# Kernel tuning notes

Hardware: AMD Instinct MI355X
Metric: run time of the kernel (lower is better)

The kernel has to match this reference:

```python
import jax, jax.numpy as jnp
from jax import lax
import numpy as np

T, B, I, H, O = 512, 64, 512, 1024, 512


def setup_inputs() -> dict:
    key = jax.random.key(0)
    ks = jax.random.split(key, 8)
    s_ih = 1.0 / np.sqrt(I)
    s_hh = 1.0 / np.sqrt(H)
    return {
        "x": jax.random.normal(ks[0], (T, B, I), dtype=jnp.float32),
        "hidden": jnp.zeros((1, B, H), dtype=jnp.float32),
        "W_ih": jax.random.normal(ks[1], (H, I), dtype=jnp.float32) * s_ih,
        "W_hh": jax.random.normal(ks[2], (H, H), dtype=jnp.float32) * s_hh,
        "b_ih": jax.random.normal(ks[3], (H,), dtype=jnp.float32) * s_hh,
        "b_hh": jax.random.normal(ks[4], (H,), dtype=jnp.float32) * s_hh,
        "W_fc": jax.random.normal(ks[5], (O, H), dtype=jnp.float32) * s_hh,
        "b_fc": jax.random.normal(ks[6], (O,), dtype=jnp.float32) * s_hh,
    }


def reference(x, hidden, W_ih, W_hh, b_ih, b_hh, W_fc, b_fc):
    # Precompute the input projection for all timesteps as one big GEMM.
    # xp: [T, B, H]
    xp = jnp.einsum("tbi,hi->tbh", x, W_ih) + b_ih

    h0 = hidden[0]  # [B, H]

    def step(h, xt):
        # PyTorch RNN (tanh): h_t = tanh(W_ih x_t + b_ih + W_hh h_{t-1} + b_hh)
        h_new = jnp.tanh(xt + h @ W_hh.T + b_hh)
        return h_new, h_new

    h_last, hs = lax.scan(step, h0, xp)  # hs: [T, B, H]

    # fc applied to flattened [T*B, H] hidden states
    out = hs.reshape(-1, hs.shape[-1]) @ W_fc.T + b_fc  # [T*B, O]
    return out, h_last[None]  # ([T*B, O], [1, B, H])
```

## Files before the change

kernel.cpp:

```cpp
#include <hip/hip_runtime.h>

typedef __attribute__((ext_vector_type(8))) short bf16x8;
typedef __attribute__((ext_vector_type(4))) float f32x4;

#define T_N 512
#define I_N 512
#define H_N 1024
#define O_N 512
#define NCL 4
#define NMEM 16
#define NTHR 512
#define COLS_H 64
#define KW 192
#define AP_STRIDE 1544
#define RST 9
#define CANARY 0xFFFFFFFFu
#define HS_CAP 20000000
#define POLL_CAP 200000

__device__ __forceinline__ unsigned short f2bf(float f) {
  unsigned int u = __float_as_uint(f);
  u += 0x7fffu + ((u >> 16) & 1u);
  return (unsigned short)(u >> 16);
}
__device__ __forceinline__ bf16x8 cvt8f(const float* __restrict__ p) {
  float4 a = *(const float4*)p;
  float4 b = *(const float4*)(p + 4);
  bf16x8 r;
  r[0] = (short)f2bf(a.x); r[1] = (short)f2bf(a.y);
  r[2] = (short)f2bf(a.z); r[3] = (short)f2bf(a.w);
  r[4] = (short)f2bf(b.x); r[5] = (short)f2bf(b.y);
  r[6] = (short)f2bf(b.z); r[7] = (short)f2bf(b.w);
  return r;
}
__device__ __forceinline__ bf16x8 cvt8v(float4 a, float4 b) {
  bf16x8 r;
  r[0] = (short)f2bf(a.x); r[1] = (short)f2bf(a.y);
  r[2] = (short)f2bf(a.z); r[3] = (short)f2bf(a.w);
  r[4] = (short)f2bf(b.x); r[5] = (short)f2bf(b.y);
  r[6] = (short)f2bf(b.z); r[7] = (short)f2bf(b.w);
  return r;
}

__device__ __forceinline__ void barrier_lds() {
  asm volatile("s_waitcnt lgkmcnt(0)" ::: "memory");
  __builtin_amdgcn_s_barrier();
  __builtin_amdgcn_sched_barrier(0);
}

__device__ __forceinline__ void st_sc01(unsigned int* p, unsigned int v) {
  asm volatile("global_store_dword %0, %1, off sc0 sc1" :: "v"(p), "v"(v) : "memory");
}
__device__ __forceinline__ void st_raw32(unsigned int* p, unsigned int v) {
  asm volatile("global_store_dword %0, %1, off" :: "v"(p), "v"(v) : "memory");
}
__device__ __forceinline__ unsigned int ld_sc01(const unsigned int* p) {
  unsigned int r;
  asm volatile("global_load_dword %0, %1, off sc0 sc1\n\ts_waitcnt vmcnt(0)"
               : "=v"(r) : "v"(p) : "memory");
  return r;
}
__device__ __forceinline__ void ld_sc01_rw(unsigned int* d, const unsigned int* p) {
  asm volatile("global_load_dword %0, %1, off sc0 sc1" : "+v"(*d) : "v"(p) : "memory");
}
__device__ __forceinline__ void ld_sc01_nw(unsigned int* d, const unsigned int* p) {
  asm volatile("global_load_dword %0, %1, off sc0 sc1" : "=v"(*d) : "v"(p) : "memory");
}
__device__ __forceinline__ void ld4_rawf(float4* d, const void* p) {
  asm volatile("global_load_dwordx4 %0, %1, off" : "=v"(*d) : "v"(p) : "memory");
}

#define PHASE(G, X0, X1, X2, X3)                                               \
  {                                                                            \
    const bool doSweep = !((G) == 0 && t == 0) && !((G) == 1 && t == T_N - 1); \
    unsigned int sw[8];                                                        \
    const unsigned int* spd = ringc;                                           \
    if (doSweep) {                                                             \
      const int swt = t - 1 + (G);                                             \
      spd = ringc + (((G) ^ 1) * 4 + (swt & 3)) * 4096 + tid;                  \
      _Pragma("unroll")                                                        \
      for (int j = 0; j < 8; ++j) {                                            \
        sw[j] = CANARY;                                                        \
        ld_sc01_rw(&sw[j], spd + 512 * j);                                     \
      }                                                                        \
    }                                                                          \
                     \
    f32x4 acc0 = {}, acc1 = {}, acc2 = {}, acc3 = {};                          \
    const int abase = (l & 15) * AP_STRIDE + wv * KW + ((l >> 4) << 3);        \
    _Pragma("unroll")                                                          \
    for (int kst = 0; kst < 6; ++kst) {                                        \
      bf16x8 a = *(const bf16x8*)(Apan + abase + kst * 32);                    \
      acc0 = __builtin_amdgcn_mfma_f32_16x16x32_bf16(a, Bh[kst][0], acc0,0,0,0);\
      acc1 = __builtin_amdgcn_mfma_f32_16x16x32_bf16(a, Bh[kst][1], acc1,0,0,0);\
      acc2 = __builtin_amdgcn_mfma_f32_16x16x32_bf16(a, Bh[kst][2], acc2,0,0,0);\
      acc3 = __builtin_amdgcn_mfma_f32_16x16x32_bf16(a, Bh[kst][3], acc3,0,0,0);\
    }                                                                          \
    if ((l >> 5) == (G)) {      \
      const int rb = ((l >> 4) & 1) << 2;                                      \
      *(f32x4*)(R + (size_t)(wv * COLS_H +  0 + (l & 15)) * RST + rb) = acc0;  \
      *(f32x4*)(R + (size_t)(wv * COLS_H + 16 + (l & 15)) * RST + rb) = acc1;  \
      *(f32x4*)(R + (size_t)(wv * COLS_H + 32 + (l & 15)) * RST + rb) = acc2;  \
      *(f32x4*)(R + (size_t)(wv * COLS_H + 48 + (l & 15)) * RST + rb) = acc3;  \
    }                                                                          \
    barrier_lds();            \
    if (wv < 4) {                                                              \
      float v0 = pb0, v1 = pb1;                                                \
      _Pragma("unroll")                                                        \
      for (int kk = 0; kk < 8; ++kk) {                                         \
        v0 += R[(size_t)(kk * COLS_H + 2 * rcp)     * RST + rrow];             \
        v1 += R[(size_t)(kk * COLS_H + 2 * rcp + 1) * RST + rrow];             \
      }                                                                        \
      const float h0 = tanhf(v0), h1 = tanhf(v1);                              \
      const unsigned int pk =                                                  \
          (unsigned int)f2bf(h0) | ((unsigned int)f2bf(h1) << 16);             \
                             \
      st_sc01(ringc + ((G) * 4 + (t & 3)) * 4096 + pubdw, pk);                 \
      st_sc01(ringc + ((G) * 4 + ((t + 2) & 3)) * 4096 + pubdw, CANARY);       \
      st_raw32((unsigned int*)(hs + ((size_t)t * 64 + b0 + (G) * 8 + rrow) * H_N \
                               + cbh + 2 * rcp), pk);                          \
      if (doSweep) {                                                           \
        asm volatile("s_waitcnt vmcnt(3)" ::: "memory");                       \
        __builtin_amdgcn_sched_barrier(0);                                     \
        bool bad = false;                                                      \
        _Pragma("unroll")                                                      \
        for (int j = 0; j < 8; ++j) bad |= (sw[j] == CANARY);                  \
        if (bad) {                                                             \
          int it = 0;                                                          \
          do {                                                                 \
            _Pragma("unroll")                                                  \
            for (int j = 0; j < 8; ++j) ld_sc01_nw(&sw[j], spd + 512 * j);     \
            asm volatile("s_waitcnt vmcnt(0)" ::: "memory");                   \
            __builtin_amdgcn_sched_barrier(0);                                 \
            bad = false;                                                       \
            _Pragma("unroll")                                                  \
            for (int j = 0; j < 8; ++j) bad |= (sw[j] == CANARY);              \
          } while (bad && ++it < POLL_CAP);                                    \
        }                                                                      \
      }                                                                        \
      if (t == T_N - 1) {                                                      \
        float2 fv; fv.x = h0; fv.y = h1;                                       \
        *(float2*)(hlast + (size_t)(b0 + (G) * 8 + rrow) * H_N + cbh + 2 * rcp) = fv; \
      }                                                                        \
    } else {                                                                   \
      if (t + 1 < T_N) {   \
        const int u = tid & 255;                                               \
        *(bf16x8*)(Apan + ((G) * 8 + (u >> 6)) * AP_STRIDE + H_N + ((u & 63) << 3)) = \
            cvt8v(X0, X1);                                                     \
        *(bf16x8*)(Apan + ((G) * 8 + (u >> 6) + 4) * AP_STRIDE + H_N + ((u & 63) << 3)) = \
            cvt8v(X2, X3);                                                     \
      }                                                                        \
      int nIss = 0;                                                            \
      if (t + 2 < T_N) {                               \
        const int u = tid & 255;                                               \
        const float* px = x + ((size_t)(t + 2) * 64 + b0 + (G) * 8 + (u >> 6)) * I_N \
                          + ((u & 63) << 3);                                   \
        ld4_rawf(&X0, px); ld4_rawf(&X1, px + 4);                              \
        ld4_rawf(&X2, px + 4 * I_N); ld4_rawf(&X3, px + 4 * I_N + 4);          \
        nIss = 4;                                                              \
      }                                                                        \
      if (doSweep) {                                                           \
        if (nIss) asm volatile("s_waitcnt vmcnt(4)" ::: "memory");             \
        else      asm volatile("s_waitcnt vmcnt(0)" ::: "memory");             \
        __builtin_amdgcn_sched_barrier(0);                                     \
        bool bad = false;                                                      \
        _Pragma("unroll")                                                      \
        for (int j = 0; j < 8; ++j) bad |= (sw[j] == CANARY);                  \
        if (bad) {                                                             \
          int it = 0;                                                          \
          do {                                                                 \
            _Pragma("unroll")                                                  \
            for (int j = 0; j < 8; ++j) ld_sc01_nw(&sw[j], spd + 512 * j);     \
            asm volatile("s_waitcnt vmcnt(0)" ::: "memory");                   \
            __builtin_amdgcn_sched_barrier(0);                                 \
            bad = false;                                                       \
            _Pragma("unroll")                                                  \
            for (int j = 0; j < 8; ++j) bad |= (sw[j] == CANARY);              \
          } while (bad && ++it < POLL_CAP);                                    \
        }                                                                      \
      }                                                                        \
    }                                                                          \
    if (doSweep) {     \
      _Pragma("unroll")                                                        \
      for (int j = 0; j < 8; ++j)                                              \
        *(unsigned int*)(Apan + ((((G) ^ 1) * 8) + j) * AP_STRIDE + (tid << 1)) = sw[j]; \
    }                                                                          \
    barrier_lds();                                   \
  }

__global__ __launch_bounds__(NTHR, 2) void rnn_scan(
    const float* __restrict__ x, const float* __restrict__ hidden,
    const float* __restrict__ Wih, const float* __restrict__ Whh,
    const float* __restrict__ bih, const float* __restrict__ bhh,
    unsigned short* __restrict__ hs, float* __restrict__ hlast,
    unsigned int* __restrict__ ring, unsigned int* __restrict__ flags)
{
  __shared__ __align__(16) unsigned short Apan[16 * AP_STRIDE];
  __shared__ __align__(16) float R[8 * COLS_H * RST];

  const int tid = threadIdx.x;
  const int l = tid & 63, wv = tid >> 6;
  const int bid = blockIdx.x;
  const int c = bid & 3;
  const int m = bid >> 2;
  const int b0 = c * 16;
  const int cbh = m * COLS_H;
  unsigned int* ringc = ring + (size_t)c * 2 * 4 * 4096;
  unsigned int* bar = flags + c * 64;

  bf16x8 Bh[6][4];
  {
    const int kb0 = wv * KW + ((l >> 4) << 3);
#pragma unroll
    for (int kst = 0; kst < 6; ++kst) {
      const int k = kb0 + kst * 32;
#pragma unroll
      for (int f = 0; f < 4; ++f) {
        const int col = cbh + f * 16 + (l & 15);
        const float* src = (k < H_N) ? (Whh + (size_t)col * H_N + k)
                                     : (Wih + (size_t)col * I_N + (k - H_N));
        Bh[kst][f] = cvt8f(src);
      }
    }
  }
  const int rrow = (tid >> 5) & 7;
  const int rcp  = tid & 31;
  const float pb0 = bih[cbh + 2 * rcp]     + bhh[cbh + 2 * rcp];
  const float pb1 = bih[cbh + 2 * rcp + 1] + bhh[cbh + 2 * rcp + 1];
  const int pubdw = rrow * 512 + m * 32 + rcp;

  {
    int q = tid;
#pragma unroll
    for (int i = 0; i < 4; ++i, q += NTHR) {
      const int row = q >> 7, col8 = (q & 127) << 3;
      *(bf16x8*)(Apan + row * AP_STRIDE + col8) =
          cvt8f(hidden + (size_t)(b0 + row) * H_N + col8);
    }
  }
  {
    int q = tid;
#pragma unroll
    for (int i = 0; i < 2; ++i, q += NTHR) {
      const int row = q >> 6, col8 = (q & 63) << 3;
      *(bf16x8*)(Apan + row * AP_STRIDE + H_N + col8) =
          cvt8f(x + (size_t)(b0 + row) * I_N + col8);
    }
  }
  if (tid < 256) {
#pragma unroll
    for (int s = 0; s < 8; ++s) st_sc01(ringc + s * 4096 + pubdw, CANARY);
  }
  asm volatile("s_waitcnt vmcnt(0)" ::: "memory");
  __syncthreads();
  if (tid == 0) st_sc01(&bar[m], 1u);
  if (tid < NMEM) {
    int it = 0;
    while (ld_sc01(&bar[tid]) < 1u && ++it < HS_CAP)
      if (it > 64) __builtin_amdgcn_s_sleep(1);
  }
  float4 xA0, xA1, xA2, xA3, xB0, xB1, xB2, xB3;
  if (wv >= 4) {
    const int u = tid & 255;
    const float* pa = x + (size_t)(64 + b0 + (u >> 6)) * I_N + ((u & 63) << 3);
    ld4_rawf(&xA0, pa); ld4_rawf(&xA1, pa + 4);
    ld4_rawf(&xA2, pa + 4 * I_N); ld4_rawf(&xA3, pa + 4 * I_N + 4);
    const float* pb = x + (size_t)(64 + b0 + 8 + (u >> 6)) * I_N + ((u & 63) << 3);
    ld4_rawf(&xB0, pb); ld4_rawf(&xB1, pb + 4);
    ld4_rawf(&xB2, pb + 4 * I_N); ld4_rawf(&xB3, pb + 4 * I_N + 4);
  }
  __syncthreads();

  for (int t = 0; t < T_N; ++t) {
    PHASE(0, xA0, xA1, xA2, xA3)
    PHASE(1, xB0, xB1, xB2, xB3)
  }
}

__global__ __launch_bounds__(256) void gemm_fc(const unsigned short* __restrict__ A,
                                               const unsigned short* __restrict__ Bt,
                                               const float* __restrict__ bias,
                                               float* __restrict__ C) {
  const int N = O_N, K = H_N;
  const int bm = blockIdx.x >> 2, bn = blockIdx.x & 3;
  const int l = threadIdx.x & 63, w = threadIdx.x >> 6;
  const int wr = w >> 1, wc = w & 1;
  const int row_a = bm * 128 + wr * 64 + (l & 15);
  const int row_b = bn * 128 + wc * 64 + (l & 15);
  const int koff = (l >> 4) * 8;
  f32x4 acc[4][4] = {};
  for (int k = 0; k < K; k += 32) {
    bf16x8 a[4], b[4];
#pragma unroll
    for (int i = 0; i < 4; i++)
      a[i] = *(const bf16x8*)(A + (size_t)(row_a + i * 16) * K + k + koff);
#pragma unroll
    for (int i = 0; i < 4; i++)
      b[i] = *(const bf16x8*)(Bt + (size_t)(row_b + i * 16) * K + k + koff);
#pragma unroll
    for (int i = 0; i < 4; i++)
#pragma unroll
      for (int j = 0; j < 4; j++)
        acc[i][j] = __builtin_amdgcn_mfma_f32_16x16x32_bf16(a[i], b[j], acc[i][j], 0, 0, 0);
  }
  const int orow = bm * 128 + wr * 64 + ((l >> 4) << 2);
  const int ocol = bn * 128 + wc * 64 + (l & 15);
#pragma unroll
  for (int i = 0; i < 4; i++)
#pragma unroll
    for (int j = 0; j < 4; j++) {
      const int r0 = orow + i * 16, c0 = ocol + j * 16;
      const float bv = bias[c0];
#pragma unroll
      for (int r = 0; r < 4; r++)
        C[(size_t)(r0 + r) * N + c0] = acc[i][j][r] + bv;
    }
}

__global__ __launch_bounds__(256) void cvt8(const float* __restrict__ s,
                                            unsigned short* __restrict__ d, long n) {
  long i = ((long)blockIdx.x * blockDim.x + threadIdx.x) * 8;
  if (i < n) *(bf16x8*)(d + i) = cvt8f(s + i);
}

extern "C" void kernel_launch(void* const* d_in, const int* in_sizes, int n_in,
                              void* d_out, int out_size, void* d_ws, size_t ws_size,
                              hipStream_t stream) {
  const float* x   = (const float*)d_in[0];
  const float* hid = (const float*)d_in[1];
  const float* Wih = (const float*)d_in[2];
  const float* Whh = (const float*)d_in[3];
  const float* bih = (const float*)d_in[4];
  const float* bhh = (const float*)d_in[5];
  const float* Wfc = (const float*)d_in[6];
  const float* bfc = (const float*)d_in[7];

  float* out   = (float*)d_out;
  float* hlast = out + (size_t)32768 * 512;

  unsigned int*   flags = (unsigned int*)d_ws;
  unsigned int*   ring  = (unsigned int*)((char*)d_ws + 4096);
  unsigned short* Wfcb  = (unsigned short*)((char*)d_ws + 4096 + 524288);
  unsigned short* hsb   = Wfcb + (size_t)512 * 1024;

  (void)hipMemsetAsync(flags, 0, 4096, stream);
  cvt8<<<256, 256, 0, stream>>>(Wfc, Wfcb, (long)512 * 1024);
  rnn_scan<<<64, NTHR, 0, stream>>>(x, hid, Wih, Whh, bih, bhh, hsb, hlast, ring, flags);
  gemm_fc<<<1024, 256, 0, stream>>>(hsb, Wfcb, bfc, out);
}
```

Before: 1.638 ms.

## Split recurrent step into four 4-row phases with deeper ring pipelining

Each block's 16 batch rows are now processed in four phases of 4 rows instead of two phases of 8, with a four-group ring buffer so a group's hidden state is published and consumed further ahead of its use. The reduction is restructured: 256 threads each produce one column value, packed via a lane shuffle before publishing. The x-staging loads are rotated across phases. A large LDS pad array is added, apparently to cap occupancy at one block per CU. The intent is to shorten the critical path per recurrent step by overlapping inter-block communication with MFMA work. The cost is twice as many barriers per timestep and more complex wait-count bookkeeping.

```diff
diff --git a/kernel.cpp b/kernel.cpp
--- a/kernel.cpp
+++ b/kernel.cpp
@@ -13,7 +13,7 @@
 #define COLS_H 64
 #define KW 192
 #define AP_STRIDE 1544
-#define RST 9
+#define SLOTDW 2048
 #define CANARY 0xFFFFFFFFu
 #define HS_CAP 20000000
 #define POLL_CAP 200000
@@ -70,121 +70,102 @@
   asm volatile("global_load_dwordx4 %0, %1, off" : "=v"(*d) : "v"(p) : "memory");
 }
 
-#define PHASE(G, X0, X1, X2, X3)                                               \
+#define PHASE(G, BISS, BCHK, XS0, XS1, XI0, XI1)                               \
   {                                                                            \
-    const bool doSweep = !((G) == 0 && t == 0) && !((G) == 1 && t == T_N - 1); \
-    unsigned int sw[8];                                                        \
-    const unsigned int* spd = ringc;                                           \
-    if (doSweep) {                                                             \
-      const int swt = t - 1 + (G);                                             \
-      spd = ringc + (((G) ^ 1) * 4 + (swt & 3)) * 4096 + tid;                  \
+    const bool iss  = ((G) == 0) ? (t >= 1) : (t <= 510);                      \
+    const bool chk  = ((G) == 3) ? (t <= 510) : (t >= 1);                      \
+    const int  tp   = ((G) == 0) ? (t - 1) : t;                                \
+    const int  tpp  = ((G) == 3) ? (t + 1) : t;                                \
+    const bool xiss = ((G) == 3) ? (t <= 509) : (t <= 510);                    \
+    const bool xstg = (t <= 510);                                              \
+    if (tid < 256) {                                                           \
+      if (iss) {                                                               \
+        const unsigned int* sb =                                               \
+            ringc + ((((G) + 3) & 3) * 4 + (tp & 3)) * SLOTDW + tid;           \
+        _Pragma("unroll")                                                      \
+        for (int q = 0; q < 8; ++q) {                                          \
+          BISS[q] = CANARY;                                                    \
+          ld_sc01_rw(&BISS[q], sb + 256 * q);                                  \
+        }                                                                      \
+      }                                                                        \
+    } else if (xiss) {                                                         \
+      const int u = tid & 255;                                                 \
+      const float* px = x + ((size_t)(tpp + 1) * 64 + b0 + 4 * (((G) + 1) & 3) \
+                             + (u >> 6)) * I_N + ((u & 63) << 3);              \
+      ld4_rawf(&XI0, px); ld4_rawf(&XI1, px + 4);                              \
+    }                                                                          \
+                                    \
+    {                                                                          \
+      f32x4 acc0 = {}, acc1 = {}, acc2 = {}, acc3 = {};                        \
+      const int abase = (l & 15) * AP_STRIDE + wv * KW + ((l >> 4) << 3);      \
       _Pragma("unroll")                                                        \
-      for (int j = 0; j < 8; ++j) {                                            \
-        sw[j] = CANARY;                                                        \
-        ld_sc01_rw(&sw[j], spd + 512 * j);                                     \
+      for (int kst = 0; kst < 6; ++kst) {                                      \
+        bf16x8 a = *(const bf16x8*)(Apan + abase + kst * 32);                  \
+        acc0 = __builtin_amdgcn_mfma_f32_16x16x32_bf16(a, Bh[kst][0], acc0, 0, 0, 0); \
+        acc1 = __builtin_amdgcn_mfma_f32_16x16x32_bf16(a, Bh[kst][1], acc1, 0, 0, 0); \
+        acc2 = __builtin_amdgcn_mfma_f32_16x16x32_bf16(a, Bh[kst][2], acc2, 0, 0, 0); \
+        acc3 = __builtin_amdgcn_mfma_f32_16x16x32_bf16(a, Bh[kst][3], acc3, 0, 0, 0); \
+      }                                                                        \
+      if ((l >> 4) == (G)) {             \
+        float* rb = Rbuf + wv * 256 + (l & 15) * 4;                            \
+        *(f32x4*)(rb +   0) = acc0; *(f32x4*)(rb +  64) = acc1;                \
+        *(f32x4*)(rb + 128) = acc2; *(f32x4*)(rb + 192) = acc3;                \
       }                                                                        \
     }                                                                          \
-                     \
-    f32x4 acc0 = {}, acc1 = {}, acc2 = {}, acc3 = {};                          \
-    const int abase = (l & 15) * AP_STRIDE + wv * KW + ((l >> 4) << 3);        \
-    _Pragma("unroll")                                                          \
-    for (int kst = 0; kst < 6; ++kst) {                                        \
-      bf16x8 a = *(const bf16x8*)(Apan + abase + kst * 32);                    \
-      acc0 = __builtin_amdgcn_mfma_f32_16x16x32_bf16(a, Bh[kst][0], acc0,0,0,0);\
-      acc1 = __builtin_amdgcn_mfma_f32_16x16x32_bf16(a, Bh[kst][1], acc1,0,0,0);\
-      acc2 = __builtin_amdgcn_mfma_f32_16x16x32_bf16(a, Bh[kst][2], acc2,0,0,0);\
-      acc3 = __builtin_amdgcn_mfma_f32_16x16x32_bf16(a, Bh[kst][3], acc3,0,0,0);\
-    }                                                                          \
-    if ((l >> 5) == (G)) {      \
-      const int rb = ((l >> 4) & 1) << 2;                                      \
-      *(f32x4*)(R + (size_t)(wv * COLS_H +  0 + (l & 15)) * RST + rb) = acc0;  \
-      *(f32x4*)(R + (size_t)(wv * COLS_H + 16 + (l & 15)) * RST + rb) = acc1;  \
-      *(f32x4*)(R + (size_t)(wv * COLS_H + 32 + (l & 15)) * RST + rb) = acc2;  \
-      *(f32x4*)(R + (size_t)(wv * COLS_H + 48 + (l & 15)) * RST + rb) = acc3;  \
-    }                                                                          \
-    barrier_lds();            \
-    if (wv < 4) {                                                              \
-      float v0 = pb0, v1 = pb1;                                                \
+    barrier_lds();          \
+    if (tid < 256) {                                                           \
+      float v = pbv;                                                           \
       _Pragma("unroll")                                                        \
-      for (int kk = 0; kk < 8; ++kk) {                                         \
-        v0 += R[(size_t)(kk * COLS_H + 2 * rcp)     * RST + rrow];             \
-        v1 += R[(size_t)(kk * COLS_H + 2 * rcp + 1) * RST + rrow];             \
-      }                                                                        \
-      const float h0 = tanhf(v0), h1 = tanhf(v1);                              \
-      const unsigned int pk =                                                  \
-          (unsigned int)f2bf(h0) | ((unsigned int)f2bf(h1) << 16);             \
-                             \
-      st_sc01(ringc + ((G) * 4 + (t & 3)) * 4096 + pubdw, pk);                 \
-      st_sc01(ringc + ((G) * 4 + ((t + 2) & 3)) * 4096 + pubdw, CANARY);       \
-      st_raw32((unsigned int*)(hs + ((size_t)t * 64 + b0 + (G) * 8 + rrow) * H_N \
-                               + cbh + 2 * rcp), pk);                          \
-      if (doSweep) {                                                           \
-        asm volatile("s_waitcnt vmcnt(3)" ::: "memory");                       \
+      for (int kk = 0; kk < 8; ++kk) v += Rbuf[kk * 256 + tid];                \
+      const float hval = tanhf(v);                                             \
+      const unsigned int pk16 = f2bf(hval);                                    \
+      const unsigned int oth = (unsigned int)__shfl_xor((int)pk16, 4);         \
+      if (!(tid & 4)) {                                                        \
+        const unsigned int pk = pk16 | (oth << 16);                            \
+        const int dwi = (tid & 3) * 512 + m * 32 + (tid >> 3);                 \
+        st_sc01(ringc + ((G) * 4 + (t & 3)) * SLOTDW + dwi, pk);               \
+        st_sc01(ringc + ((G) * 4 + ((t + 2) & 3)) * SLOTDW + dwi, CANARY);     \
+        st_raw32((unsigned int*)hs +                                           \
+                 ((size_t)t * 64 + b0 + 4 * (G) + (tid & 3)) * 512 +           \
+                 m * 32 + (tid >> 3), pk);                                     \
+      }                                                                        \
+      if (t == T_N - 1)                                                        \
+        hlast[(size_t)(b0 + 4 * (G) + (tid & 3)) * H_N + cbh + (tid >> 2)] = hval; \
+      if (chk) {                                                               \
+        asm volatile("s_waitcnt vmcnt(25)" ::: "memory");                      \
         __builtin_amdgcn_sched_barrier(0);                                     \
         bool bad = false;                                                      \
         _Pragma("unroll")                                                      \
-        for (int j = 0; j < 8; ++j) bad |= (sw[j] == CANARY);                  \
-        if (bad) {                                                             \
-          int it = 0;                                                          \
+        for (int q = 0; q < 8; ++q) bad |= (BCHK[q] == CANARY);                \
+        if (bad) {    \
+          const int ts = ((G) == 3) ? t : (t - 1);                             \
+          const unsigned int* sb2 =                                            \
+              ringc + ((((G) + 1) & 3) * 4 + (ts & 3)) * SLOTDW + tid;         \
+          int itc = 0;                                                         \
           do {                                                                 \
             _Pragma("unroll")                                                  \
-            for (int j = 0; j < 8; ++j) ld_sc01_nw(&sw[j], spd + 512 * j);     \
+            for (int q = 0; q < 8; ++q) ld_sc01_nw(&BCHK[q], sb2 + 256 * q);   \
             asm volatile("s_waitcnt vmcnt(0)" ::: "memory");                   \
             __builtin_amdgcn_sched_barrier(0);                                 \
             bad = false;                                                       \
             _Pragma("unroll")                                                  \
-            for (int j = 0; j < 8; ++j) bad |= (sw[j] == CANARY);              \
-          } while (bad && ++it < POLL_CAP);                                    \
+            for (int q = 0; q < 8; ++q) bad |= (BCHK[q] == CANARY);            \
+          } while (bad && ++itc < POLL_CAP);                                   \
         }                                                                      \
-      }                                                                        \
-      if (t == T_N - 1) {                                                      \
-        float2 fv; fv.x = h0; fv.y = h1;                                       \
-        *(float2*)(hlast + (size_t)(b0 + (G) * 8 + rrow) * H_N + cbh + 2 * rcp) = fv; \
-      }                                                                        \
-    } else {                                                                   \
-      if (t + 1 < T_N) {   \
-        const int u = tid & 255;                                               \
-        *(bf16x8*)(Apan + ((G) * 8 + (u >> 6)) * AP_STRIDE + H_N + ((u & 63) << 3)) = \
-            cvt8v(X0, X1);                                                     \
-        *(bf16x8*)(Apan + ((G) * 8 + (u >> 6) + 4) * AP_STRIDE + H_N + ((u & 63) << 3)) = \
-            cvt8v(X2, X3);                                                     \
-      }                                                                        \
-      int nIss = 0;                                                            \
-      if (t + 2 < T_N) {                               \
-        const int u = tid & 255;                                               \
-        const float* px = x + ((size_t)(t + 2) * 64 + b0 + (G) * 8 + (u >> 6)) * I_N \
-                          + ((u & 63) << 3);                                   \
-        ld4_rawf(&X0, px); ld4_rawf(&X1, px + 4);                              \
-        ld4_rawf(&X2, px + 4 * I_N); ld4_rawf(&X3, px + 4 * I_N + 4);          \
-        nIss = 4;                                                              \
-      }                                                                        \
-      if (doSweep) {                                                           \
-        if (nIss) asm volatile("s_waitcnt vmcnt(4)" ::: "memory");             \
-        else      asm volatile("s_waitcnt vmcnt(0)" ::: "memory");             \
-        __builtin_amdgcn_sched_barrier(0);                                     \
-        bool bad = false;                                                      \
         _Pragma("unroll")                                                      \
-        for (int j = 0; j < 8; ++j) bad |= (sw[j] == CANARY);                  \
-        if (bad) {                                                             \
-          int it = 0;                                                          \
-          do {                                                                 \
-            _Pragma("unroll")                                                  \
-            for (int j = 0; j < 8; ++j) ld_sc01_nw(&sw[j], spd + 512 * j);     \
-            asm volatile("s_waitcnt vmcnt(0)" ::: "memory");                   \
-            __builtin_amdgcn_sched_barrier(0);                                 \
-            bad = false;                                                       \
-            _Pragma("unroll")                                                  \
-            for (int j = 0; j < 8; ++j) bad |= (sw[j] == CANARY);              \
-          } while (bad && ++it < POLL_CAP);                                    \
-        }                                                                      \
-      }                                                                        \
+        for (int q = 0; q < 8; ++q)                                            \
+          *(unsigned int*)(Apan + (4 * (((G) + 1) & 3) + (q >> 1)) * AP_STRIDE \
+                           + ((tid + ((q & 1) << 8)) << 1)) = BCHK[q];         \
+      }                                                                        \
+    } else if (xstg) {                                                         \
+      if (xiss) asm volatile("s_waitcnt vmcnt(2)" ::: "memory");               \
+      else      asm volatile("s_waitcnt vmcnt(0)" ::: "memory");               \
+      __builtin_amdgcn_sched_barrier(0);                                       \
+      const int u = tid & 255;                                                 \
+      *(bf16x8*)(Apan + (4 * (G) + (u >> 6)) * AP_STRIDE + H_N + ((u & 63) << 3)) \
+          = cvt8v(XS0, XS1);                                                   \
     }                                                                          \
-    if (doSweep) {     \
-      _Pragma("unroll")                                                        \
-      for (int j = 0; j < 8; ++j)                                              \
-        *(unsigned int*)(Apan + ((((G) ^ 1) * 8) + j) * AP_STRIDE + (tid << 1)) = sw[j]; \
-    }                                                                          \
-    barrier_lds();                                   \
+    barrier_lds();                    \
   }
 
 __global__ __launch_bounds__(NTHR, 2) void rnn_scan(
@@ -195,7 +176,8 @@
     unsigned int* __restrict__ ring, unsigned int* __restrict__ flags)
 {
   __shared__ __align__(16) unsigned short Apan[16 * AP_STRIDE];
-  __shared__ __align__(16) float R[8 * COLS_H * RST];
+  __shared__ __align__(16) float Rbuf[8 * 256];
+  __shared__ char pad_[24576];
 
   const int tid = threadIdx.x;
   const int l = tid & 63, wv = tid >> 6;
@@ -204,8 +186,9 @@
   const int m = bid >> 2;
   const int b0 = c * 16;
   const int cbh = m * COLS_H;
-  unsigned int* ringc = ring + (size_t)c * 2 * 4 * 4096;
+  unsigned int* ringc = ring + (size_t)c * 4 * 4 * SLOTDW;
   unsigned int* bar = flags + c * 64;
+  if (x == nullptr) pad_[0] = 1;
 
   bf16x8 Bh[6][4];
   {
@@ -222,11 +205,8 @@
       }
     }
   }
-  const int rrow = (tid >> 5) & 7;
-  const int rcp  = tid & 31;
-  const float pb0 = bih[cbh + 2 * rcp]     + bhh[cbh + 2 * rcp];
-  const float pb1 = bih[cbh + 2 * rcp + 1] + bhh[cbh + 2 * rcp + 1];
-  const int pubdw = rrow * 512 + m * 32 + rcp;
+  const int rcol = (tid < 256) ? (tid >> 2) : 0;
+  const float pbv = bih[cbh + rcol] + bhh[cbh + rcol];
 
   {
     int q = tid;
@@ -246,9 +226,10 @@
           cvt8f(x + (size_t)(b0 + row) * I_N + col8);
     }
   }
-  if (tid < 256) {
-#pragma unroll
-    for (int s = 0; s < 8; ++s) st_sc01(ringc + s * 4096 + pubdw, CANARY);
+  if (tid < 256 && !(tid & 4)) {
+    const int dwi = (tid & 3) * 512 + m * 32 + (tid >> 3);
+#pragma unroll
+    for (int s = 0; s < 16; ++s) st_sc01(ringc + s * SLOTDW + dwi, CANARY);
   }
   asm volatile("s_waitcnt vmcnt(0)" ::: "memory");
   __syncthreads();
@@ -258,21 +239,20 @@
     while (ld_sc01(&bar[tid]) < 1u && ++it < HS_CAP)
       if (it > 64) __builtin_amdgcn_s_sleep(1);
   }
-  float4 xA0, xA1, xA2, xA3, xB0, xB1, xB2, xB3;
+  float4 XA0, XA1, XB0, XB1;
   if (wv >= 4) {
     const int u = tid & 255;
-    const float* pa = x + (size_t)(64 + b0 + (u >> 6)) * I_N + ((u & 63) << 3);
-    ld4_rawf(&xA0, pa); ld4_rawf(&xA1, pa + 4);
-    ld4_rawf(&xA2, pa + 4 * I_N); ld4_rawf(&xA3, pa + 4 * I_N + 4);
-    const float* pb = x + (size_t)(64 + b0 + 8 + (u >> 6)) * I_N + ((u & 63) << 3);
-    ld4_rawf(&xB0, pb); ld4_rawf(&xB1, pb + 4);
-    ld4_rawf(&xB2, pb + 4 * I_N); ld4_rawf(&xB3, pb + 4 * I_N + 4);
+    const float* px = x + ((size_t)64 + b0 + (u >> 6)) * I_N + ((u & 63) << 3);
+    ld4_rawf(&XA0, px); ld4_rawf(&XA1, px + 4);
   }
   __syncthreads();
 
+  unsigned int sw0[8], sw1[8], sw2[8], sw3[8];
   for (int t = 0; t < T_N; ++t) {
-    PHASE(0, xA0, xA1, xA2, xA3)
-    PHASE(1, xB0, xB1, xB2, xB3)
+    PHASE(0, sw0, sw2, XA0, XA1, XB0, XB1)
+    PHASE(1, sw1, sw3, XB0, XB1, XA0, XA1)
+    PHASE(2, sw2, sw0, XA0, XA1, XB0, XB1)
+    PHASE(3, sw3, sw1, XB0, XB1, XA0, XA1)
   }
 }
 
```

Result: slower. 3.119 ms (+90.4%).

## Fuse output FC projection into recurrent scan kernel, dropping separate GEMM

Applied to the files above, without the earlier changes.

Each persistent scan block now also holds a slice of W_fc in registers and, at each step, computes the FC output for the previous timestep's hidden state from the Apan tile it has already staged. Results are written directly to the output. This removes the hs bf16 buffer, the W_fc conversion kernel and the separate FC GEMM launch. In exchange the serial critical path of every timestep carries extra MFMA work, LDS reductions and output stores, and an epilogue is added to handle the last timestep.

```diff
diff --git a/kernel.cpp b/kernel.cpp
--- a/kernel.cpp
+++ b/kernel.cpp
@@ -12,6 +12,7 @@
 #define NTHR 512
 #define COLS_H 64
 #define KW 192
+#define KWFC 128
 #define AP_STRIDE 1544
 #define RST 9
 #define CANARY 0xFFFFFFFFu
@@ -72,7 +73,7 @@
 
 #define PHASE(G, X0, X1, X2, X3)                                               \
   {                                                                            \
-    const bool doSweep = !((G) == 0 && t == 0) && !((G) == 1 && t == T_N - 1); \
+    const bool doSweep = !((G) == 0 && t == 0);                                \
     unsigned int sw[8];                                                        \
     const unsigned int* spd = ringc;                                           \
     if (doSweep) {                                                             \
@@ -84,23 +85,41 @@
         ld_sc01_rw(&sw[j], spd + 512 * j);                                     \
       }                                                                        \
     }                                                                          \
-                     \
-    f32x4 acc0 = {}, acc1 = {}, acc2 = {}, acc3 = {};                          \
-    const int abase = (l & 15) * AP_STRIDE + wv * KW + ((l >> 4) << 3);        \
-    _Pragma("unroll")                                                          \
-    for (int kst = 0; kst < 6; ++kst) {                                        \
-      bf16x8 a = *(const bf16x8*)(Apan + abase + kst * 32);                    \
-      acc0 = __builtin_amdgcn_mfma_f32_16x16x32_bf16(a, Bh[kst][0], acc0,0,0,0);\
-      acc1 = __builtin_amdgcn_mfma_f32_16x16x32_bf16(a, Bh[kst][1], acc1,0,0,0);\
-      acc2 = __builtin_amdgcn_mfma_f32_16x16x32_bf16(a, Bh[kst][2], acc2,0,0,0);\
-      acc3 = __builtin_amdgcn_mfma_f32_16x16x32_bf16(a, Bh[kst][3], acc3,0,0,0);\
-    }                                                                          \
-    if ((l >> 5) == (G)) {      \
-      const int rb = ((l >> 4) & 1) << 2;                                      \
-      *(f32x4*)(R + (size_t)(wv * COLS_H +  0 + (l & 15)) * RST + rb) = acc0;  \
-      *(f32x4*)(R + (size_t)(wv * COLS_H + 16 + (l & 15)) * RST + rb) = acc1;  \
-      *(f32x4*)(R + (size_t)(wv * COLS_H + 32 + (l & 15)) * RST + rb) = acc2;  \
-      *(f32x4*)(R + (size_t)(wv * COLS_H + 48 + (l & 15)) * RST + rb) = acc3;  \
+          \
+    {                                                                          \
+      f32x4 acc0 = {}, acc1 = {}, acc2 = {}, acc3 = {};                        \
+      const int abase = (l & 15) * AP_STRIDE + wv * KW + ((l >> 4) << 3);      \
+      _Pragma("unroll")                                                        \
+      for (int kst = 0; kst < 6; ++kst) {                                      \
+        bf16x8 a = *(const bf16x8*)(Apan + abase + kst * 32);                  \
+        acc0 = __builtin_amdgcn_mfma_f32_16x16x32_bf16(a, Bh[kst][0], acc0,0,0,0);\
+        acc1 = __builtin_amdgcn_mfma_f32_16x16x32_bf16(a, Bh[kst][1], acc1,0,0,0);\
+        acc2 = __builtin_amdgcn_mfma_f32_16x16x32_bf16(a, Bh[kst][2], acc2,0,0,0);\
+        acc3 = __builtin_amdgcn_mfma_f32_16x16x32_bf16(a, Bh[kst][3], acc3,0,0,0);\
+      }                                                                        \
+      if ((l >> 5) == (G)) {    \
+        const int rb = ((l >> 4) & 1) << 2;                                    \
+        *(f32x4*)(R + (size_t)(wv * COLS_H +  0 + (l & 15)) * RST + rb) = acc0;\
+        *(f32x4*)(R + (size_t)(wv * COLS_H + 16 + (l & 15)) * RST + rb) = acc1;\
+        *(f32x4*)(R + (size_t)(wv * COLS_H + 32 + (l & 15)) * RST + rb) = acc2;\
+        *(f32x4*)(R + (size_t)(wv * COLS_H + 48 + (l & 15)) * RST + rb) = acc3;\
+      }                                                                        \
+    }                                                                          \
+        \
+    if (t > 0) {                                                               \
+      f32x4 afc0 = {}, afc1 = {};                                              \
+      const int ab2 = (l & 15) * AP_STRIDE + wv * KWFC + ((l >> 4) << 3);      \
+      _Pragma("unroll")                                                        \
+      for (int kst = 0; kst < 4; ++kst) {                                      \
+        bf16x8 a = *(const bf16x8*)(Apan + ab2 + kst * 32);                    \
+        afc0 = __builtin_amdgcn_mfma_f32_16x16x32_bf16(a, Bf[kst][0], afc0,0,0,0);\
+        afc1 = __builtin_amdgcn_mfma_f32_16x16x32_bf16(a, Bf[kst][1], afc1,0,0,0);\
+      }                                                                        \
+      if ((l >> 5) == (G)) {                                                   \
+        const int rb = ((l >> 4) & 1) << 2;                                    \
+        *(f32x4*)(R2 + (size_t)(wv * 32 +      (l & 15)) * RST + rb) = afc0;   \
+        *(f32x4*)(R2 + (size_t)(wv * 32 + 16 + (l & 15)) * RST + rb) = afc1;   \
+      }                                                                        \
     }                                                                          \
     barrier_lds();            \
     if (wv < 4) {                                                              \
@@ -110,16 +129,25 @@
         v0 += R[(size_t)(kk * COLS_H + 2 * rcp)     * RST + rrow];             \
         v1 += R[(size_t)(kk * COLS_H + 2 * rcp + 1) * RST + rrow];             \
       }                                                                        \
+      float vfc = bfv;                                                         \
+      if (t > 0) {                                                             \
+        _Pragma("unroll")                                                      \
+        for (int kk = 0; kk < 8; ++kk)                                         \
+          vfc += R2[(size_t)(kk * 32 + rcp) * RST + rrow];                     \
+      }                                                                        \
       const float h0 = tanhf(v0), h1 = tanhf(v1);                              \
       const unsigned int pk =                                                  \
           (unsigned int)f2bf(h0) | ((unsigned int)f2bf(h1) << 16);             \
-                             \
+                                \
       st_sc01(ringc + ((G) * 4 + (t & 3)) * 4096 + pubdw, pk);                 \
       st_sc01(ringc + ((G) * 4 + ((t + 2) & 3)) * 4096 + pubdw, CANARY);       \
-      st_raw32((unsigned int*)(hs + ((size_t)t * 64 + b0 + (G) * 8 + rrow) * H_N \
-                               + cbh + 2 * rcp), pk);                          \
+      if (t > 0)                                                               \
+        st_raw32((unsigned int*)out +                                          \
+                 ((size_t)(t - 1) * 64 + b0 + (G) * 8 + rrow) * O_N            \
+                 + cbfc + rcp, __float_as_uint(vfc));                          \
       if (doSweep) {                                                           \
-        asm volatile("s_waitcnt vmcnt(3)" ::: "memory");                       \
+        if (t > 0) asm volatile("s_waitcnt vmcnt(3)" ::: "memory");            \
+        else       asm volatile("s_waitcnt vmcnt(2)" ::: "memory");            \
         __builtin_amdgcn_sched_barrier(0);                                     \
         bool bad = false;                                                      \
         _Pragma("unroll")                                                      \
@@ -142,7 +170,7 @@
         *(float2*)(hlast + (size_t)(b0 + (G) * 8 + rrow) * H_N + cbh + 2 * rcp) = fv; \
       }                                                                        \
     } else {                                                                   \
-      if (t + 1 < T_N) {   \
+      if (t + 1 < T_N) {      \
         const int u = tid & 255;                                               \
         *(bf16x8*)(Apan + ((G) * 8 + (u >> 6)) * AP_STRIDE + H_N + ((u & 63) << 3)) = \
             cvt8v(X0, X1);                                                     \
@@ -187,15 +215,17 @@
     barrier_lds();                                   \
   }
 
-__global__ __launch_bounds__(NTHR, 2) void rnn_scan(
+__global__ __launch_bounds__(NTHR, 2) void rnn_fused(
     const float* __restrict__ x, const float* __restrict__ hidden,
     const float* __restrict__ Wih, const float* __restrict__ Whh,
     const float* __restrict__ bih, const float* __restrict__ bhh,
-    unsigned short* __restrict__ hs, float* __restrict__ hlast,
+    const float* __restrict__ Wfc, const float* __restrict__ bfc,
+    float* __restrict__ out, float* __restrict__ hlast,
     unsigned int* __restrict__ ring, unsigned int* __restrict__ flags)
 {
   __shared__ __align__(16) unsigned short Apan[16 * AP_STRIDE];
-  __shared__ __align__(16) float R[8 * COLS_H * RST];
+  __shared__ __align__(16) float R [8 * COLS_H * RST];
+  __shared__ __align__(16) float R2[8 * 32 * RST];
 
   const int tid = threadIdx.x;
   const int l = tid & 63, wv = tid >> 6;
@@ -204,6 +234,7 @@
   const int m = bid >> 2;
   const int b0 = c * 16;
   const int cbh = m * COLS_H;
+  const int cbfc = m * 32;
   unsigned int* ringc = ring + (size_t)c * 2 * 4 * 4096;
   unsigned int* bar = flags + c * 64;
 
@@ -222,10 +253,20 @@
       }
     }
   }
+  bf16x8 Bf[4][2];
+  {
+    const int kb0 = wv * KWFC + ((l >> 4) << 3);
+#pragma unroll
+    for (int kst = 0; kst < 4; ++kst)
+#pragma unroll
+      for (int f = 0; f < 2; ++f)
+        Bf[kst][f] = cvt8f(Wfc + (size_t)(cbfc + f * 16 + (l & 15)) * H_N + kb0 + kst * 32);
+  }
   const int rrow = (tid >> 5) & 7;
   const int rcp  = tid & 31;
   const float pb0 = bih[cbh + 2 * rcp]     + bhh[cbh + 2 * rcp];
   const float pb1 = bih[cbh + 2 * rcp + 1] + bhh[cbh + 2 * rcp + 1];
+  const float bfv = bfc[cbfc + rcp];
   const int pubdw = rrow * 512 + m * 32 + rcp;
 
   {
@@ -274,52 +315,52 @@
     PHASE(0, xA0, xA1, xA2, xA3)
     PHASE(1, xB0, xB1, xB2, xB3)
   }
-}
-
-__global__ __launch_bounds__(256) void gemm_fc(const unsigned short* __restrict__ A,
-                                               const unsigned short* __restrict__ Bt,
-                                               const float* __restrict__ bias,
-                                               float* __restrict__ C) {
-  const int N = O_N, K = H_N;
-  const int bm = blockIdx.x >> 2, bn = blockIdx.x & 3;
-  const int l = threadIdx.x & 63, w = threadIdx.x >> 6;
-  const int wr = w >> 1, wc = w & 1;
-  const int row_a = bm * 128 + wr * 64 + (l & 15);
-  const int row_b = bn * 128 + wc * 64 + (l & 15);
-  const int koff = (l >> 4) * 8;
-  f32x4 acc[4][4] = {};
-  for (int k = 0; k < K; k += 32) {
-    bf16x8 a[4], b[4];
-#pragma unroll
-    for (int i = 0; i < 4; i++)
-      a[i] = *(const bf16x8*)(A + (size_t)(row_a + i * 16) * K + k + koff);
-#pragma unroll
-    for (int i = 0; i < 4; i++)
-      b[i] = *(const bf16x8*)(Bt + (size_t)(row_b + i * 16) * K + k + koff);
-#pragma unroll
-    for (int i = 0; i < 4; i++)
-#pragma unroll
-      for (int j = 0; j < 4; j++)
-        acc[i][j] = __builtin_amdgcn_mfma_f32_16x16x32_bf16(a[i], b[j], acc[i][j], 0, 0, 0);
-  }
-  const int orow = bm * 128 + wr * 64 + ((l >> 4) << 2);
-  const int ocol = bn * 128 + wc * 64 + (l & 15);
-#pragma unroll
-  for (int i = 0; i < 4; i++)
-#pragma unroll
-    for (int j = 0; j < 4; j++) {
-      const int r0 = orow + i * 16, c0 = ocol + j * 16;
-      const float bv = bias[c0];
-#pragma unroll
-      for (int r = 0; r < 4; r++)
-        C[(size_t)(r0 + r) * N + c0] = acc[i][j][r] + bv;
-    }
-}
-
-__global__ __launch_bounds__(256) void cvt8(const float* __restrict__ s,
-                                            unsigned short* __restrict__ d, long n) {
-  long i = ((long)blockIdx.x * blockDim.x + threadIdx.x) * 8;
-  if (i < n) *(bf16x8*)(d + i) = cvt8f(s + i);
+
+  {
+    const unsigned int* sp = ringc + (1 * 4 + (511 & 3)) * 4096 + tid;
+    unsigned int sw[8];
+    int it = 0; bool bad;
+    do {
+#pragma unroll
+      for (int j = 0; j < 8; ++j) ld_sc01_nw(&sw[j], sp + 512 * j);
+      asm volatile("s_waitcnt vmcnt(0)" ::: "memory");
+      __builtin_amdgcn_sched_barrier(0);
+      bad = false;
+#pragma unroll
+      for (int j = 0; j < 8; ++j) bad |= (sw[j] == CANARY);
+    } while (bad && ++it < POLL_CAP);
+#pragma unroll
+    for (int j = 0; j < 8; ++j)
+      *(unsigned int*)(Apan + (8 + j) * AP_STRIDE + (tid << 1)) = sw[j];
+  }
+  __syncthreads();
+  {
+    f32x4 afc0 = {}, afc1 = {};
+    const int ab2 = (l & 15) * AP_STRIDE + wv * KWFC + ((l >> 4) << 3);
+#pragma unroll
+    for (int kst = 0; kst < 4; ++kst) {
+      bf16x8 a = *(const bf16x8*)(Apan + ab2 + kst * 32);
+      afc0 = __builtin_amdgcn_mfma_f32_16x16x32_bf16(a, Bf[kst][0], afc0, 0, 0, 0);
+      afc1 = __builtin_amdgcn_mfma_f32_16x16x32_bf16(a, Bf[kst][1], afc1, 0, 0, 0);
+    }
+#pragma unroll
+    for (int g = 0; g < 2; ++g) {
+      if ((l >> 5) == g) {
+        const int rb = ((l >> 4) & 1) << 2;
+        *(f32x4*)(R2 + (size_t)(wv * 32 +      (l & 15)) * RST + rb) = afc0;
+        *(f32x4*)(R2 + (size_t)(wv * 32 + 16 + (l & 15)) * RST + rb) = afc1;
+      }
+      __syncthreads();
+      if (tid < 256) {
+        float vfc = bfv;
+#pragma unroll
+        for (int kk = 0; kk < 8; ++kk)
+          vfc += R2[(size_t)(kk * 32 + rcp) * RST + rrow];
+        out[((size_t)511 * 64 + b0 + g * 8 + rrow) * O_N + cbfc + rcp] = vfc;
+      }
+      __syncthreads();
+    }
+  }
 }
 
 extern "C" void kernel_launch(void* const* d_in, const int* in_sizes, int n_in,
@@ -337,13 +378,10 @@
   float* out   = (float*)d_out;
   float* hlast = out + (size_t)32768 * 512;
 
-  unsigned int*   flags = (unsigned int*)d_ws;
-  unsigned int*   ring  = (unsigned int*)((char*)d_ws + 4096);
-  unsigned short* Wfcb  = (unsigned short*)((char*)d_ws + 4096 + 524288);
-  unsigned short* hsb   = Wfcb + (size_t)512 * 1024;
+  unsigned int* flags = (unsigned int*)d_ws;
+  unsigned int* ring  = (unsigned int*)((char*)d_ws + 4096);
 
   (void)hipMemsetAsync(flags, 0, 4096, stream);
-  cvt8<<<256, 256, 0, stream>>>(Wfc, Wfcb, (long)512 * 1024);
-  rnn_scan<<<64, NTHR, 0, stream>>>(x, hid, Wih, Whh, bih, bhh, hsb, hlast, ring, flags);
-  gemm_fc<<<1024, 256, 0, stream>>>(hsb, Wfcb, bfc, out);
-}
+  rnn_fused<<<64, NTHR, 0, stream>>>(x, hid, Wih, Whh, bih, bhh, Wfc, bfc,
+                                     out, hlast, ring, flags);
+}
```

Result: slower. 2.390 ms (+45.9%).
